# Kernel optimization log

Measured on AMD Instinct MI355X. Metric: run time of the kernel, lower is better.

Reference implementation:

```python
import jax, jax.numpy as jnp
import numpy as np

B, T, VOCAB = 8192, 1024, 10000

def setup_inputs() -> dict:
    key = jax.random.key(0)
    k1, k2, k3, k4 = jax.random.split(key, 4)
    sample_seq = jax.random.randint(k1, (B, T), 0, VOCAB, dtype=jnp.int32)
    sample_seqLogprobs = jax.random.normal(k2, (B, T), dtype=jnp.float32)
    sample_value = jax.random.normal(k3, (B, T), dtype=jnp.float32)
    sample_reward = jax.random.normal(k4, (B, T), dtype=jnp.float32)
    return {
        "sample_seq": sample_seq,
        "sample_seqLogprobs": sample_seqLogprobs,
        "sample_value": sample_value,
        "sample_reward": sample_reward,
    }

def reference(sample_seq, sample_seqLogprobs, sample_value, sample_reward):
    # Vectorized version of the per-element python loop: zero out every token
    # at or after the first EOS (token id 0). cumsum>0 of the EOS indicator is
    # the running-max (cummax) of (seq==0).
    at_or_after_eos = jnp.cumsum((sample_seq == 0).astype(jnp.int32), axis=1) > 0
    seq = jnp.where(at_or_after_eos, 0, sample_seq)  # [B, T]

    # mask = (seq>0), shifted right by one with a leading column of ones
    mask = (seq > 0).astype(sample_seqLogprobs.dtype)
    mask = jnp.concatenate(
        [jnp.ones((mask.shape[0], 1), mask.dtype), mask[:, :-1]], axis=1
    )

    # sample_reward is a detached numpy array in the original (no grad)
    reward = jax.lax.stop_gradient(sample_reward)
    reward_diff = reward - sample_value  # [B, T]

    # masked REINFORCE loss, normalized by number of valid tokens
    output = -sample_seqLogprobs * reward_diff * mask
    loss = output.sum() / mask.sum()
    return loss
```

## Files before the change

### kernel.cpp

```cpp
#include <hip/hip_runtime.h>

#define BROWS 8192
#define TLEN  1024

__global__ __launch_bounds__(256) void row_reduce_kernel(
    const int*   __restrict__ seq,
    const float* __restrict__ logp,
    const float* __restrict__ value,
    const float* __restrict__ reward,
    double*      __restrict__ row_sum,
    double*      __restrict__ row_cnt)
{
    const int b   = blockIdx.x;
    const int tid = threadIdx.x;
    const int lane = tid & 63;
    const int wave = tid >> 6;

    const size_t rowoff = (size_t)b * TLEN;
    const int4*   s4 = (const int4*)  (seq    + rowoff);
    const float4* l4 = (const float4*)(logp   + rowoff);
    const float4* v4 = (const float4*)(value  + rowoff);
    const float4* r4 = (const float4*)(reward + rowoff);

    const int4   s = s4[tid];
    const float4 l = l4[tid];
    const float4 v = v4[tid];
    const float4 r = r4[tid];

    const int base = tid * 4;

    int fz = TLEN;
    if (s.w == 0) fz = base + 3;
    if (s.z == 0) fz = base + 2;
    if (s.y == 0) fz = base + 1;
    if (s.x == 0) fz = base + 0;

    #pragma unroll
    for (int off = 32; off > 0; off >>= 1)
        fz = min(fz, __shfl_down(fz, off, 64));

    __shared__ int    lds_fz[4];
    __shared__ double lds_sum[4];
    if (lane == 0) lds_fz[wave] = fz;
    __syncthreads();
    const int block_fz = min(min(lds_fz[0], lds_fz[1]),
                             min(lds_fz[2], lds_fz[3]));

    double acc = 0.0;
    if (base + 0 <= block_fz) acc += (double)(-l.x * (r.x - v.x));
    if (base + 1 <= block_fz) acc += (double)(-l.y * (r.y - v.y));
    if (base + 2 <= block_fz) acc += (double)(-l.z * (r.z - v.z));
    if (base + 3 <= block_fz) acc += (double)(-l.w * (r.w - v.w));

    #pragma unroll
    for (int off = 32; off > 0; off >>= 1)
        acc += __shfl_down(acc, off, 64);

    if (lane == 0) lds_sum[wave] = acc;
    __syncthreads();
    if (tid == 0) {
        row_sum[b] = lds_sum[0] + lds_sum[1] + lds_sum[2] + lds_sum[3];
        row_cnt[b] = (double)min(block_fz + 1, TLEN);
    }
}

__global__ __launch_bounds__(256) void final_reduce_kernel(
    const double* __restrict__ row_sum,
    const double* __restrict__ row_cnt,
    float*        __restrict__ out)
{
    const int tid  = threadIdx.x;
    const int lane = tid & 63;
    const int wave = tid >> 6;

    double s = 0.0, c = 0.0;
    for (int i = tid; i < BROWS; i += 256) {
        s += row_sum[i];
        c += row_cnt[i];
    }
    #pragma unroll
    for (int off = 32; off > 0; off >>= 1) {
        s += __shfl_down(s, off, 64);
        c += __shfl_down(c, off, 64);
    }
    __shared__ double ls[4], lc[4];
    if (lane == 0) { ls[wave] = s; lc[wave] = c; }
    __syncthreads();
    if (tid == 0) {
        double ts = ls[0] + ls[1] + ls[2] + ls[3];
        double tc = lc[0] + lc[1] + lc[2] + lc[3];
        out[0] = (float)(ts / tc);
    }
}

extern "C" void kernel_launch(void* const* d_in, const int* in_sizes, int n_in,
                              void* d_out, int out_size, void* d_ws, size_t ws_size,
                              hipStream_t stream) {
    const int*   seq    = (const int*)  d_in[0];
    const float* logp   = (const float*)d_in[1];
    const float* value  = (const float*)d_in[2];
    const float* reward = (const float*)d_in[3];
    float* out = (float*)d_out;

    double* row_sum = (double*)d_ws;
    double* row_cnt = row_sum + BROWS;

    row_reduce_kernel<<<BROWS, 256, 0, stream>>>(seq, logp, value, reward,
                                                 row_sum, row_cnt);
    final_reduce_kernel<<<1, 256, 0, stream>>>(row_sum, row_cnt, out);
}
```

Baseline: 153.1 us.

## Map one wavefront per row to drop LDS and block barriers

Each 64-lane wavefront now processes a whole row, loading four float4/int4 chunks per lane, instead of a 256-thread block per row. The first-EOS min reduction and the partial-sum reduction stay entirely in-wave, so the shared-memory staging and both __syncthreads are removed, and the grid shrinks fourfold. Shuffles switch from shfl_down to shfl_xor. The cost is more registers per thread and more loads in flight per lane. The kernel stays memory-bound on a roughly 128 MB read.

```diff
diff --git a/kernel.cpp b/kernel.cpp
--- a/kernel.cpp
+++ b/kernel.cpp
@@ -11,56 +11,57 @@
     double*      __restrict__ row_sum,
     double*      __restrict__ row_cnt)
 {
-    const int b   = blockIdx.x;
-    const int tid = threadIdx.x;
-    const int lane = tid & 63;
-    const int wave = tid >> 6;
+    const int row  = blockIdx.x * 4 + (threadIdx.x >> 6);
+    const int lane = threadIdx.x & 63;
 
-    const size_t rowoff = (size_t)b * TLEN;
+    const size_t rowoff = (size_t)row * TLEN;
     const int4*   s4 = (const int4*)  (seq    + rowoff);
     const float4* l4 = (const float4*)(logp   + rowoff);
     const float4* v4 = (const float4*)(value  + rowoff);
     const float4* r4 = (const float4*)(reward + rowoff);
 
-    const int4   s = s4[tid];
-    const float4 l = l4[tid];
-    const float4 v = v4[tid];
-    const float4 r = r4[tid];
-
-    const int base = tid * 4;
+    int4   s[4];
+    float4 l[4], v[4], r[4];
+    #pragma unroll
+    for (int k = 0; k < 4; ++k) {
+        const int idx = k * 64 + lane;
+        s[k] = s4[idx];
+        l[k] = l4[idx];
+        v[k] = v4[idx];
+        r[k] = r4[idx];
+    }
 
     int fz = TLEN;
-    if (s.w == 0) fz = base + 3;
-    if (s.z == 0) fz = base + 2;
-    if (s.y == 0) fz = base + 1;
-    if (s.x == 0) fz = base + 0;
+    #pragma unroll
+    for (int k = 3; k >= 0; --k) {
+        const int base = k * 256 + lane * 4;
+        if (s[k].w == 0) fz = base + 3;
+        if (s[k].z == 0) fz = base + 2;
+        if (s[k].y == 0) fz = base + 1;
+        if (s[k].x == 0) fz = base + 0;
+    }
 
     #pragma unroll
     for (int off = 32; off > 0; off >>= 1)
-        fz = min(fz, __shfl_down(fz, off, 64));
-
-    __shared__ int    lds_fz[4];
-    __shared__ double lds_sum[4];
-    if (lane == 0) lds_fz[wave] = fz;
-    __syncthreads();
-    const int block_fz = min(min(lds_fz[0], lds_fz[1]),
-                             min(lds_fz[2], lds_fz[3]));
+        fz = min(fz, __shfl_xor(fz, off, 64));
 
     double acc = 0.0;
-    if (base + 0 <= block_fz) acc += (double)(-l.x * (r.x - v.x));
-    if (base + 1 <= block_fz) acc += (double)(-l.y * (r.y - v.y));
-    if (base + 2 <= block_fz) acc += (double)(-l.z * (r.z - v.z));
-    if (base + 3 <= block_fz) acc += (double)(-l.w * (r.w - v.w));
+    #pragma unroll
+    for (int k = 0; k < 4; ++k) {
+        const int base = k * 256 + lane * 4;
+        if (base + 0 <= fz) acc += (double)(-l[k].x * (r[k].x - v[k].x));
+        if (base + 1 <= fz) acc += (double)(-l[k].y * (r[k].y - v[k].y));
+        if (base + 2 <= fz) acc += (double)(-l[k].z * (r[k].z - v[k].z));
+        if (base + 3 <= fz) acc += (double)(-l[k].w * (r[k].w - v[k].w));
+    }
 
     #pragma unroll
     for (int off = 32; off > 0; off >>= 1)
-        acc += __shfl_down(acc, off, 64);
+        acc += __shfl_xor(acc, off, 64);
 
-    if (lane == 0) lds_sum[wave] = acc;
-    __syncthreads();
-    if (tid == 0) {
-        row_sum[b] = lds_sum[0] + lds_sum[1] + lds_sum[2] + lds_sum[3];
-        row_cnt[b] = (double)min(block_fz + 1, TLEN);
+    if (lane == 0) {
+        row_sum[row] = acc;
+        row_cnt[row] = (double)min(fz + 1, TLEN);
     }
 }
 
@@ -80,8 +81,8 @@
     }
     #pragma unroll
     for (int off = 32; off > 0; off >>= 1) {
-        s += __shfl_down(s, off, 64);
-        c += __shfl_down(c, off, 64);
+        s += __shfl_xor(s, off, 64);
+        c += __shfl_xor(c, off, 64);
     }
     __shared__ double ls[4], lc[4];
     if (lane == 0) { ls[wave] = s; lc[wave] = c; }
@@ -105,7 +106,7 @@
     double* row_sum = (double*)d_ws;
     double* row_cnt = row_sum + BROWS;
 
-    row_reduce_kernel<<<BROWS, 256, 0, stream>>>(seq, logp, value, reward,
-                                                 row_sum, row_cnt);
+    row_reduce_kernel<<<BROWS / 4, 256, 0, stream>>>(seq, logp, value, reward,
+                                                     row_sum, row_cnt);
     final_reduce_kernel<<<1, 256, 0, stream>>>(row_sum, row_cnt, out);
 }
```

After: 156.5 us. +2.2%, slower.
